# Performance work log

Measured on AMD Instinct MI355X. Metric: run time of the kernel, lower is better.

Reference implementation:

```python
import jax, jax.numpy as jnp
import numpy as np

B, S, D, H = 4, 2048, 512, 8
DK = D // H

def setup_inputs() -> dict:
    key = jax.random.key(0)
    ks = jax.random.split(key, 16)
    w = lambda i, shp: (jax.random.normal(ks[i], shp, jnp.float32) * 0.02)
    return {
        "q": jax.random.normal(ks[0], (B, S, D), jnp.float32),
        "k": jax.random.normal(ks[1], (B, S, D), jnp.float32),
        "v": jax.random.normal(ks[2], (B, S, D), jnp.float32),
        "mask": jax.random.randint(ks[3], (B, 1, S), 0, 2, jnp.int32),
        "Lexicon": jax.random.uniform(ks[4], (B, S), jnp.float32) * 1000.0,
        "Wq": w(5, (D, D)), "bq": w(6, (D,)),
        "Wk": w(7, (D, D)), "bk": w(8, (D,)),
        "Wv": w(9, (D, D)), "bv": w(10, (D,)),
        "Wo": w(11, (D, D)), "bo": w(12, (D,)),
        "Wl": w(13, (S, S)), "bl": w(14, (S,)),
    }

def reference(q, k, v, mask, Lexicon, Wq, bq, Wk, bk, Wv, bv, Wo, bo, Wl, bl):
    NEG = jnp.float32(-1e9)
    proj = lambda x, W, b: (x @ W + b).reshape(B, S, H, DK).transpose(0, 2, 1, 3)  # [B,H,S,DK]
    qh, kh, vh = proj(q, Wq, bq), proj(k, Wk, bk), proj(v, Wv, bv)
    scores = jnp.einsum('bhqd,bhkd->bhqk', qh, kh) / jnp.sqrt(jnp.float32(DK))  # [B,H,S,S]
    lex = (Lexicon / 1000.0) @ Wl + bl  # [B,S] lexicon bias over key positions
    m = mask[:, None, :, :] == 1  # [B,1,1,S]
    scores = jnp.where(m, NEG, scores)
    lexb = jnp.where(m, NEG, lex[:, None, None, :])  # [B,1,1,S]; broadcast over heads & queries
    # dropout in eval mode (identity); dual softmax then average
    attn = (jax.nn.softmax(scores, axis=-1) + jax.nn.softmax(lexb, axis=-1)) * 0.5
    out = jnp.einsum('bhqk,bhkd->bhqd', attn, vh)
    concat = out.transpose(0, 2, 1, 3).reshape(B, S, D)
    return concat @ Wo + bo
```

## Files before the change

kernel.cpp:

```cpp
#include <hip/hip_runtime.h>


typedef __attribute__((ext_vector_type(4))) float f32x4;
typedef __attribute__((ext_vector_type(8))) short s16x8;
typedef __attribute__((ext_vector_type(4))) short s16x4;

#define QSCALE 0.18033688011112042f

__device__ inline short f2bf(float f) {
  __bf16 h = (__bf16)f;
  return __builtin_bit_cast(short, h);
}
__device__ inline float fast_exp2(float x) {
#if __has_builtin(__builtin_amdgcn_exp2f)
  return __builtin_amdgcn_exp2f(x);
#else
  return exp2f(x);
#endif
}
__device__ inline void gl_lds16(const void* g, void* l) {
  __builtin_amdgcn_global_load_lds(
      (const __attribute__((address_space(1))) void*)g,
      (__attribute__((address_space(3))) void*)l, 16, 0, 0);
}

struct PrepArgs {
  const float* W[4];
  short* WT[4];
  const float* Lex;
  const float* Wl;
  float* part;
};

__global__ __launch_bounds__(256) void prep(PrepArgs pa) {
  const int blk = blockIdx.x;
  if (blk < 1024) {
    const int z = blk >> 8, tt = blk & 255;
    const float* __restrict__ W = pa.W[z];
    short* __restrict__ WT = pa.WT[z];
    const int n0 = (tt & 15) * 32, k0 = (tt >> 4) * 32;
    const int tx = threadIdx.x & 31, ty = threadIdx.x >> 5;
    __shared__ float Tl[32][33];
#pragma unroll
    for (int j = 0; j < 4; ++j)
      Tl[ty + j * 8][tx] = W[(size_t)(k0 + ty + j * 8) * 512 + n0 + tx];
    __syncthreads();
#pragma unroll
    for (int j = 0; j < 4; ++j) {
      int n = n0 + ty + j * 8, k = k0 + tx;
      int kg = k >> 3;
      int kswz = (((kg & ~7) | ((kg & 7) ^ (n & 7))) << 3) | (k & 7);
      WT[(size_t)n * 512 + kswz] = f2bf(Tl[tx][ty + j * 8]);
    }
  } else {
    const int jb = blk - 1024;
    const int j = (jb & 7) * 256 + threadIdx.x;
    const int sb = jb >> 3, s0 = sb * 128;
    __shared__ float Lsh[4][128];
#pragma unroll
    for (int l = 0; l < 2; ++l) {
      int idx = threadIdx.x + l * 256;
      Lsh[idx >> 7][idx & 127] = pa.Lex[(idx >> 7) * 2048 + s0 + (idx & 127)];
    }
    __syncthreads();
    float a0 = 0.f, a1 = 0.f, a2 = 0.f, a3 = 0.f;
#pragma unroll 4
    for (int si = 0; si < 128; ++si) {
      float w = pa.Wl[(size_t)(s0 + si) * 2048 + j];
      a0 += Lsh[0][si] * w; a1 += Lsh[1][si] * w;
      a2 += Lsh[2][si] * w; a3 += Lsh[3][si] * w;
    }
    pa.part[(sb * 4 + 0) * 2048 + j] = a0;
    pa.part[(sb * 4 + 1) * 2048 + j] = a1;
    pa.part[(sb * 4 + 2) * 2048 + j] = a2;
    pa.part[(sb * 4 + 3) * 2048 + j] = a3;
  }
}

__global__ __launch_bounds__(256) void plex_exp(const float* __restrict__ part,
                                                const float* __restrict__ bl,
                                                const int* __restrict__ mask,
                                                float* __restrict__ expv,
                                                float* __restrict__ psum) {
  const int b = blockIdx.x >> 3, jb = blockIdx.x & 7;
  const int j = jb * 256 + threadIdx.x;
  float s = 0.f;
#pragma unroll
  for (int sb = 0; sb < 16; ++sb) s += part[(sb * 4 + b) * 2048 + j];
  float vv = s * 0.001f + bl[j];
  float e = (mask[b * 2048 + j] == 1) ? 0.f : __expf(vv);
  expv[b * 2048 + j] = e;
  __shared__ float red[256];
  red[threadIdx.x] = e;
  __syncthreads();
  for (int off = 128; off; off >>= 1) {
    if (threadIdx.x < off) red[threadIdx.x] += red[threadIdx.x + off];
    __syncthreads();
  }
  if (threadIdx.x == 0) psum[b * 8 + jb] = red[0];
}

__global__ __launch_bounds__(256) void vbar1(const float* __restrict__ v,
                                             const float* __restrict__ expv,
                                             float* __restrict__ t1p) {
  const int blk = blockIdx.x;
  const int b = blk >> 6, kb = blk & 63;
  const int tid = threadIdx.x;
  float a0 = 0.f, a1 = 0.f;
#pragma unroll 4
  for (int kk = 0; kk < 32; ++kk) {
    int k = kb * 32 + kk;
    float e = expv[b * 2048 + k];
    const float* vr = v + (size_t)(b * 2048 + k) * 512;
    a0 += e * vr[tid];
    a1 += e * vr[tid + 256];
  }
  t1p[(size_t)blk * 512 + tid] = a0;
  t1p[(size_t)blk * 512 + tid + 256] = a1;
}

__global__ __launch_bounds__(256) void vbar2(const float* __restrict__ t1p,
                                             const float* __restrict__ psum,
                                             const float* __restrict__ Wv,
                                             const float* __restrict__ bv,
                                             float* __restrict__ vbar) {
  const int b = blockIdx.x, jb = blockIdx.y, tid = threadIdx.x;
  const int jl = tid & 63, sp = tid >> 6;
  const int j = jb * 64 + jl;
  __shared__ float t1[512];
  __shared__ float red[4][64];
#pragma unroll
  for (int l = 0; l < 2; ++l) {
    int idx = tid + l * 256;
    float s = 0.f;
#pragma unroll 8
    for (int p = 0; p < 64; ++p) s += t1p[(size_t)(b * 64 + p) * 512 + idx];
    t1[idx] = s;
  }
  __syncthreads();
  float a = 0.f;
#pragma unroll 4
  for (int d = sp * 128; d < sp * 128 + 128; ++d) a += t1[d] * Wv[(size_t)d * 512 + j];
  red[sp][jl] = a;
  __syncthreads();
  if (sp == 0) {
    float tot = 0.f;
#pragma unroll
    for (int p = 0; p < 8; ++p) tot += psum[b * 8 + p];
    float s = red[0][jl] + red[1][jl] + red[2][jl] + red[3][jl];
    vbar[b * 512 + j] = s / tot + bv[j];
  }
}

struct GemmArgs {
  const void* X[3];
  const short* WT[3];
  const float* bias[3];
  void* C[3];
  float oscale[3];
  int mode[3];
  const int* mask;
};

template <bool IN_F32>
__global__ __launch_bounds__(256) void gemm_fused(GemmArgs ga) {
  constexpr int LDA = IN_F32 ? 72 : 64;
  __shared__ alignas(16) short SH[64 * 72 + 128 * 64];
  short* Al = SH;
  short* Bl = SH + 64 * LDA;
  const int t = blockIdx.z;
  const short* __restrict__ WT = ga.WT[t];
  const float* __restrict__ bias = ga.bias[t];
  const int tid = threadIdx.x;
  const int lane = tid & 63, wid = tid >> 6;
  const int lr = lane & 15, lg = lane >> 4;
  const int wm = wid >> 1, wn = wid & 1;
  const int m0 = blockIdx.x * 64, n0 = blockIdx.y * 128;
  const int grow = lane >> 3, gch = lane & 7;

  f32x4 acc[2][4];
#pragma unroll
  for (int i = 0; i < 2; ++i)
#pragma unroll
    for (int j = 0; j < 4; ++j) acc[i][j] = {0.f, 0.f, 0.f, 0.f};

  for (int k0 = 0; k0 < 512; k0 += 64) {
    __syncthreads();
    if constexpr (IN_F32) {
      const float* X = (const float*)ga.X[t];
#pragma unroll
      for (int ii = 0; ii < 4; ++ii) {
        int fidx = tid + ii * 256;
        int row = fidx >> 4, kq = fidx & 15;
        f32x4 vv = *(const f32x4*)(X + (size_t)(m0 + row) * 512 + k0 + kq * 4);
        s16x4 hv = {f2bf(vv[0]), f2bf(vv[1]), f2bf(vv[2]), f2bf(vv[3])};
        *(s16x4*)(&Al[row * 72 + kq * 4]) = hv;
      }
    } else {
      const short* X = (const short*)ga.X[t];
#pragma unroll
      for (int c = 0; c < 2; ++c) {
        int r0 = wid * 16 + c * 8;
        int row = r0 + grow;
        gl_lds16(X + (size_t)(m0 + row) * 512 + k0 + ((gch ^ (row & 7)) << 3),
                 &Al[r0 * 64]);
      }
    }
#pragma unroll
    for (int c = 0; c < 4; ++c) {
      int r0 = wid * 32 + c * 8;
      int row = r0 + grow;
      gl_lds16(WT + (size_t)(n0 + row) * 512 + k0 + (gch << 3), &Bl[r0 * 64]);
    }
    __syncthreads();
#pragma unroll
    for (int ks = 0; ks < 2; ++ks) {
      s16x8 a[2], bfr[4];
#pragma unroll
      for (int mt = 0; mt < 2; ++mt) {
        int m = wm * 32 + mt * 16 + lr;
        if constexpr (IN_F32)
          a[mt] = *(const s16x8*)(&Al[m * 72 + ks * 32 + lg * 8]);
        else
          a[mt] = *(const s16x8*)(&Al[m * 64 + (((ks * 4 + lg) ^ (m & 7)) << 3)]);
      }
#pragma unroll
      for (int nt = 0; nt < 4; ++nt) {
        int n = wn * 64 + nt * 16 + lr;
        bfr[nt] = *(const s16x8*)(&Bl[n * 64 + (((ks * 4 + lg) ^ (n & 7)) << 3)]);
      }
#pragma unroll
      for (int mt = 0; mt < 2; ++mt)
#pragma unroll
        for (int nt = 0; nt < 4; ++nt)
          acc[mt][nt] = __builtin_amdgcn_mfma_f32_16x16x32_bf16(a[mt], bfr[nt],
                                                                acc[mt][nt], 0, 0, 0);
    }
  }
  const float os = ga.oscale[t];
  const int mode = ga.mode[t];
  if (mode == 1) {
    __syncthreads();
    short* Tt = SH;
#pragma unroll
    for (int nt = 0; nt < 4; ++nt) {
      int dl = wn * 64 + nt * 16 + lr;
      float bvv = bias[n0 + dl];
#pragma unroll
      for (int mt = 0; mt < 2; ++mt) {
        int sl = wm * 32 + mt * 16 + lg * 4;
#pragma unroll
        for (int i = 0; i < 4; ++i) {
          float mf = (ga.mask[m0 + sl + i] == 1) ? 0.f : 1.f;
          Tt[dl * 72 + sl + i] = f2bf((acc[mt][nt][i] + bvv) * mf);
        }
      }
    }
    __syncthreads();
    const int dl = tid >> 1, sh = (tid & 1) * 32;
    const int n = n0 + dl;
    const size_t base =
        ((size_t)((m0 >> 11) * 8 + (n >> 6)) * 64 + (n & 63)) * 2048 +
        (m0 & 2047) + sh;
#pragma unroll
    for (int c = 0; c < 4; ++c)
      *(s16x8*)((short*)ga.C[t] + base + c * 8) =
          *(const s16x8*)(&Tt[dl * 72 + sh + c * 8]);
  } else {
#pragma unroll
    for (int nt = 0; nt < 4; ++nt) {
      int col = n0 + wn * 64 + nt * 16 + lr;
      float bvv = bias[col];
#pragma unroll
      for (int mt = 0; mt < 2; ++mt) {
        int r0 = m0 + wm * 32 + mt * 16 + lg * 4;
        if (mode == 2) {
#pragma unroll
          for (int i = 0; i < 4; ++i)
            ((float*)ga.C[t])[(size_t)(r0 + i) * 512 + col] = acc[mt][nt][i] + bvv;
        } else {
#pragma unroll
          for (int i = 0; i < 4; ++i)
            ((short*)ga.C[t])[(size_t)(r0 + i) * 512 + col] =
                f2bf((acc[mt][nt][i] + bvv) * os);
        }
      }
    }
  }
}

__global__ __launch_bounds__(512) void flash_attn(const short* __restrict__ Qp,
                                                  const short* __restrict__ Kp,
                                                  const short* __restrict__ Vt,
                                                  const int* __restrict__ mask,
                                                  const float* __restrict__ vbar,
                                                  short* __restrict__ concat) {
  constexpr int S = 2048;
  __shared__ alignas(16) short Kl[2][64 * 72];
  __shared__ alignas(16) short Vl[2][64 * 72];
  __shared__ alignas(16) short Pl[8][16 * 72];
  __shared__ alignas(16) short Mb[2][64];
  const int id = blockIdx.x;
  const int xcd = id & 7, iw = id >> 3;
  const int bh = xcd * 4 + (iw >> 4), qb = iw & 15;
  const int b = bh >> 3, h = bh & 7;
  const int q0 = qb * 128;
  const int tid = threadIdx.x;
  const int lane = tid & 63, wid = tid >> 6;
  const int lr = lane & 15, lg = lane >> 4;

  const short* Qbase = Qp + ((size_t)(b * S) + q0 + wid * 16 + lr) * 512 + h * 64;
  const s16x8 aq0 = *(const s16x8*)(Qbase + lg * 8);
  const s16x8 aq1 = *(const s16x8*)(Qbase + 32 + lg * 8);

  const int srow = tid >> 3, sc = tid & 7;
  const short* Kg = Kp + ((size_t)(b * S) + srow) * 512 + h * 64 + sc * 8;
  const short* Vg = Vt + ((size_t)(bh * 64) + srow) * 2048 + sc * 8;

  s16x8 kreg = *(const s16x8*)(Kg);
  s16x8 vreg = *(const s16x8*)(Vg);
  *(s16x8*)(&Kl[0][srow * 72 + sc * 8]) = kreg;
  *(s16x8*)(&Vl[0][srow * 72 + sc * 8]) = vreg;
  if (tid < 64) Mb[0][tid] = (mask[b * S + tid] == 1) ? (short)0 : (short)0x3F80;
  __syncthreads();

  f32x4 acc[4];
#pragma unroll
  for (int i = 0; i < 4; ++i) acc[i] = {0.f, 0.f, 0.f, 0.f};
  f32x4 accL = {0.f, 0.f, 0.f, 0.f};
  const f32x4 zero = {0.f, 0.f, 0.f, 0.f};

  int cur = 0;
  for (int t = 0; t < 32; ++t) {
    const int nxt = cur ^ 1;
    int mnxt = 0;
    if (t < 31) {
      const size_t kv0n = (size_t)(t + 1) * 64;
      kreg = *(const s16x8*)(Kg + kv0n * 512);
      vreg = *(const s16x8*)(Vg + kv0n);
      if (tid < 64) mnxt = mask[b * S + kv0n + tid];
    }
    f32x4 st[4];
#pragma unroll
    for (int nt = 0; nt < 4; ++nt) {
      s16x8 k0f = *(const s16x8*)(&Kl[cur][(nt * 16 + lr) * 72 + lg * 8]);
      s16x8 k1f = *(const s16x8*)(&Kl[cur][(nt * 16 + lr) * 72 + 32 + lg * 8]);
      f32x4 tt = __builtin_amdgcn_mfma_f32_16x16x32_bf16(k0f, aq0, zero, 0, 0, 0);
      st[nt] = __builtin_amdgcn_mfma_f32_16x16x32_bf16(k1f, aq1, tt, 0, 0, 0);
    }
#pragma unroll
    for (int nt = 0; nt < 4; ++nt) {
      float p0 = fast_exp2(st[nt][0]);
      float p1 = fast_exp2(st[nt][1]);
      float p2 = fast_exp2(st[nt][2]);
      float p3 = fast_exp2(st[nt][3]);
      s16x4 pk = {f2bf(p0), f2bf(p1), f2bf(p2), f2bf(p3)};
      *(s16x4*)(&Pl[wid][lr * 72 + nt * 16 + lg * 4]) = pk;
    }
#pragma unroll
    for (int ks = 0; ks < 2; ++ks) {
      s16x8 ap = *(const s16x8*)(&Pl[wid][lr * 72 + ks * 32 + lg * 8]);
      s16x8 bm = *(const s16x8*)(&Mb[cur][ks * 32 + lg * 8]);
      accL = __builtin_amdgcn_mfma_f32_16x16x32_bf16(ap, bm, accL, 0, 0, 0);
#pragma unroll
      for (int dt = 0; dt < 4; ++dt) {
        s16x8 bv = *(const s16x8*)(&Vl[cur][(dt * 16 + lr) * 72 + ks * 32 + lg * 8]);
        acc[dt] = __builtin_amdgcn_mfma_f32_16x16x32_bf16(ap, bv, acc[dt], 0, 0, 0);
      }
    }
    if (t < 31) {
      *(s16x8*)(&Kl[nxt][srow * 72 + sc * 8]) = kreg;
      *(s16x8*)(&Vl[nxt][srow * 72 + sc * 8]) = vreg;
      if (tid < 64) Mb[nxt][tid] = (mnxt == 1) ? (short)0 : (short)0x3F80;
    }
    __syncthreads();
    cur = nxt;
  }
  f32x4 linv;
#pragma unroll
  for (int i = 0; i < 4; ++i) linv[i] = 0.5f / accL[i];
#pragma unroll
  for (int dt = 0; dt < 4; ++dt) {
    int d = dt * 16 + lr;
    float vb = 0.5f * vbar[bh * 64 + d];
#pragma unroll
    for (int i = 0; i < 4; ++i) {
      int q = q0 + wid * 16 + lg * 4 + i;
      concat[((size_t)(b * S) + q) * 512 + h * 64 + d] =
          f2bf(acc[dt][i] * linv[i] + vb);
    }
  }
}

extern "C" void kernel_launch(void* const* d_in, const int* in_sizes, int n_in,
                              void* d_out, int out_size, void* d_ws, size_t ws_size,
                              hipStream_t stream) {
  const float* q    = (const float*)d_in[0];
  const float* k    = (const float*)d_in[1];
  const float* v    = (const float*)d_in[2];
  const int*   mask = (const int*)d_in[3];
  const float* Lex  = (const float*)d_in[4];
  const float* Wq   = (const float*)d_in[5];
  const float* bq   = (const float*)d_in[6];
  const float* Wk   = (const float*)d_in[7];
  const float* bk   = (const float*)d_in[8];
  const float* Wv   = (const float*)d_in[9];
  const float* bv   = (const float*)d_in[10];
  const float* Wo   = (const float*)d_in[11];
  const float* bo   = (const float*)d_in[12];
  const float* Wl   = (const float*)d_in[13];
  const float* bl   = (const float*)d_in[14];
  float* out = (float*)d_out;

  char* ws = (char*)d_ws;
  const size_t TSZ = (size_t)8192 * 512 * 2;
  short* Qp  = (short*)(ws);
  short* Kp  = (short*)(ws + TSZ);
  short* Vtp = (short*)(ws + 2 * TSZ);
  short* Cc  = (short*)(ws + 3 * TSZ);
  float* part = (float*)(ws + 3 * TSZ);
  float* t1p  = (float*)(ws + 3 * TSZ + (512 << 10));
  short* WTq = (short*)(ws + 4 * TSZ);
  short* WTk = WTq + 512 * 512;
  short* WTv = WTk + 512 * 512;
  short* WTo = WTv + 512 * 512;
  float* expv  = (float*)(ws + 4 * TSZ + 4 * 512 * 512 * 2);
  float* psum  = expv + 4 * 2048;
  float* vbarp = psum + 64;

  PrepArgs pa;
  pa.W[0] = Wq; pa.W[1] = Wk; pa.W[2] = Wv; pa.W[3] = Wo;
  pa.WT[0] = WTq; pa.WT[1] = WTk; pa.WT[2] = WTv; pa.WT[3] = WTo;
  pa.Lex = Lex; pa.Wl = Wl; pa.part = part;
  prep<<<1152, 256, 0, stream>>>(pa);

  plex_exp<<<32, 256, 0, stream>>>(part, bl, mask, expv, psum);
  vbar1<<<256, 256, 0, stream>>>(v, expv, t1p);
  vbar2<<<dim3(4, 8), 256, 0, stream>>>(t1p, psum, Wv, bv, vbarp);

  GemmArgs gqkv;
  gqkv.X[0] = q;   gqkv.X[1] = k;   gqkv.X[2] = v;
  gqkv.WT[0] = WTq; gqkv.WT[1] = WTk; gqkv.WT[2] = WTv;
  gqkv.bias[0] = bq; gqkv.bias[1] = bk; gqkv.bias[2] = bv;
  gqkv.C[0] = Qp; gqkv.C[1] = Kp; gqkv.C[2] = Vtp;
  gqkv.oscale[0] = QSCALE; gqkv.oscale[1] = 1.f; gqkv.oscale[2] = 1.f;
  gqkv.mode[0] = 0; gqkv.mode[1] = 0; gqkv.mode[2] = 1;
  gqkv.mask = mask;
  gemm_fused<true><<<dim3(128, 4, 3), 256, 0, stream>>>(gqkv);

  flash_attn<<<512, 512, 0, stream>>>(Qp, Kp, Vtp, mask, vbarp, Cc);

  GemmArgs go;
  go.X[0] = Cc; go.WT[0] = WTo; go.bias[0] = bo; go.C[0] = out;
  go.oscale[0] = 1.f; go.mode[0] = 2;
  go.X[1] = nullptr; go.WT[1] = nullptr; go.bias[1] = nullptr; go.C[1] = nullptr;
  go.X[2] = nullptr; go.WT[2] = nullptr; go.bias[2] = nullptr; go.C[2] = nullptr;
  go.oscale[1] = go.oscale[2] = 1.f; go.mode[1] = go.mode[2] = 0;
  go.mask = mask;
  gemm_fused<false><<<dim3(128, 4, 1), 256, 0, stream>>>(go);
}
```

Before: 137.2 us.

## Fuse lexicon/vbar prep into QKV GEMM, widen GEMM N-tile, restructure flash attention

Removes the plex_exp and vbar1 kernels by running their work in an extra z-slice of the QKV GEMM launch, which cuts two launches and the expv round trip. GEMM tiles widen from 64x128 to 64x256, halving the grid and doubling per-block accumulators. Flash attention moves to 256-thread blocks that each process 32 query rows per wave, uses global_load_lds directly into XOR-swizzled unpadded LDS, and reuses K/V fragments across two query halves. The cost is higher register pressure and fewer blocks, which may lower occupancy.

```diff
diff --git a/kernel.cpp b/kernel.cpp
--- a/kernel.cpp
+++ b/kernel.cpp
@@ -77,50 +77,8 @@
   }
 }
 
-__global__ __launch_bounds__(256) void plex_exp(const float* __restrict__ part,
-                                                const float* __restrict__ bl,
-                                                const int* __restrict__ mask,
-                                                float* __restrict__ expv,
-                                                float* __restrict__ psum) {
-  const int b = blockIdx.x >> 3, jb = blockIdx.x & 7;
-  const int j = jb * 256 + threadIdx.x;
-  float s = 0.f;
-#pragma unroll
-  for (int sb = 0; sb < 16; ++sb) s += part[(sb * 4 + b) * 2048 + j];
-  float vv = s * 0.001f + bl[j];
-  float e = (mask[b * 2048 + j] == 1) ? 0.f : __expf(vv);
-  expv[b * 2048 + j] = e;
-  __shared__ float red[256];
-  red[threadIdx.x] = e;
-  __syncthreads();
-  for (int off = 128; off; off >>= 1) {
-    if (threadIdx.x < off) red[threadIdx.x] += red[threadIdx.x + off];
-    __syncthreads();
-  }
-  if (threadIdx.x == 0) psum[b * 8 + jb] = red[0];
-}
-
-__global__ __launch_bounds__(256) void vbar1(const float* __restrict__ v,
-                                             const float* __restrict__ expv,
-                                             float* __restrict__ t1p) {
-  const int blk = blockIdx.x;
-  const int b = blk >> 6, kb = blk & 63;
-  const int tid = threadIdx.x;
-  float a0 = 0.f, a1 = 0.f;
-#pragma unroll 4
-  for (int kk = 0; kk < 32; ++kk) {
-    int k = kb * 32 + kk;
-    float e = expv[b * 2048 + k];
-    const float* vr = v + (size_t)(b * 2048 + k) * 512;
-    a0 += e * vr[tid];
-    a1 += e * vr[tid + 256];
-  }
-  t1p[(size_t)blk * 512 + tid] = a0;
-  t1p[(size_t)blk * 512 + tid + 256] = a1;
-}
-
 __global__ __launch_bounds__(256) void vbar2(const float* __restrict__ t1p,
-                                             const float* __restrict__ psum,
+                                             const float* __restrict__ psp,
                                              const float* __restrict__ Wv,
                                              const float* __restrict__ bv,
                                              float* __restrict__ vbar) {
@@ -145,8 +103,8 @@
   __syncthreads();
   if (sp == 0) {
     float tot = 0.f;
-#pragma unroll
-    for (int p = 0; p < 8; ++p) tot += psum[b * 8 + p];
+#pragma unroll 8
+    for (int p = 0; p < 64; ++p) tot += psp[b * 64 + p];
     float s = red[0][jl] + red[1][jl] + red[2][jl] + red[3][jl];
     vbar[b * 512 + j] = s / tot + bv[j];
   }
@@ -160,29 +118,65 @@
   float oscale[3];
   int mode[3];
   const int* mask;
+  const float* part;
+  const float* bl;
+  const float* vsrc;
+  float* t1p;
+  float* psp;
 };
 
 template <bool IN_F32>
 __global__ __launch_bounds__(256) void gemm_fused(GemmArgs ga) {
+  __shared__ alignas(16) short SH[64 * 72 + 256 * 64];
+  const int tid = threadIdx.x;
+
+  if (blockIdx.z == 3) {
+    float* ek = (float*)SH;
+    const int id2 = blockIdx.y * 128 + blockIdx.x;
+    const int b = id2 >> 6, kb = id2 & 63;
+    if (tid < 32) {
+      int k = kb * 32 + tid;
+      float s = 0.f;
+#pragma unroll
+      for (int sb = 0; sb < 16; ++sb) s += ga.part[(sb * 4 + b) * 2048 + k];
+      float lx = s * 0.001f + ga.bl[k];
+      ek[tid] = (ga.mask[b * 2048 + k] == 1) ? 0.f : __expf(lx);
+    }
+    __syncthreads();
+    float a0 = 0.f, a1 = 0.f;
+#pragma unroll 4
+    for (int kk = 0; kk < 32; ++kk) {
+      float e = ek[kk];
+      const float* vr = ga.vsrc + (size_t)(b * 2048 + kb * 32 + kk) * 512;
+      a0 += e * vr[tid];
+      a1 += e * vr[tid + 256];
+    }
+    ga.t1p[(size_t)id2 * 512 + tid] = a0;
+    ga.t1p[(size_t)id2 * 512 + tid + 256] = a1;
+    if (tid == 0) {
+      float s = 0.f;
+      for (int i = 0; i < 32; ++i) s += ek[i];
+      ga.psp[id2] = s;
+    }
+    return;
+  }
+
   constexpr int LDA = IN_F32 ? 72 : 64;
-  __shared__ alignas(16) short SH[64 * 72 + 128 * 64];
   short* Al = SH;
   short* Bl = SH + 64 * LDA;
   const int t = blockIdx.z;
   const short* __restrict__ WT = ga.WT[t];
   const float* __restrict__ bias = ga.bias[t];
-  const int tid = threadIdx.x;
   const int lane = tid & 63, wid = tid >> 6;
   const int lr = lane & 15, lg = lane >> 4;
   const int wm = wid >> 1, wn = wid & 1;
-  const int m0 = blockIdx.x * 64, n0 = blockIdx.y * 128;
-  const int grow = lane >> 3, gch = lane & 7;
-
-  f32x4 acc[2][4];
+  const int m0 = blockIdx.x * 64, n0 = blockIdx.y * 256;
+
+  f32x4 acc[2][8];
 #pragma unroll
   for (int i = 0; i < 2; ++i)
 #pragma unroll
-    for (int j = 0; j < 4; ++j) acc[i][j] = {0.f, 0.f, 0.f, 0.f};
+    for (int j = 0; j < 8; ++j) acc[i][j] = {0.f, 0.f, 0.f, 0.f};
 
   for (int k0 = 0; k0 < 512; k0 += 64) {
     __syncthreads();
@@ -200,22 +194,22 @@
       const short* X = (const short*)ga.X[t];
 #pragma unroll
       for (int c = 0; c < 2; ++c) {
-        int r0 = wid * 16 + c * 8;
-        int row = r0 + grow;
-        gl_lds16(X + (size_t)(m0 + row) * 512 + k0 + ((gch ^ (row & 7)) << 3),
-                 &Al[r0 * 64]);
-      }
-    }
-#pragma unroll
-    for (int c = 0; c < 4; ++c) {
-      int r0 = wid * 32 + c * 8;
-      int row = r0 + grow;
-      gl_lds16(WT + (size_t)(n0 + row) * 512 + k0 + (gch << 3), &Bl[r0 * 64]);
+        int u = c * 256 + tid;
+        int row = u >> 3, g = u & 7;
+        gl_lds16(X + (size_t)(m0 + row) * 512 + k0 + ((g ^ (row & 7)) << 3),
+                 &Al[u * 8]);
+      }
+    }
+#pragma unroll
+    for (int c = 0; c < 8; ++c) {
+      int u = c * 256 + tid;
+      int row = u >> 3, g = u & 7;
+      gl_lds16(WT + (size_t)(n0 + row) * 512 + k0 + (g << 3), &Bl[u * 8]);
     }
     __syncthreads();
 #pragma unroll
     for (int ks = 0; ks < 2; ++ks) {
-      s16x8 a[2], bfr[4];
+      s16x8 a[2], bfr[8];
 #pragma unroll
       for (int mt = 0; mt < 2; ++mt) {
         int m = wm * 32 + mt * 16 + lr;
@@ -225,14 +219,14 @@
           a[mt] = *(const s16x8*)(&Al[m * 64 + (((ks * 4 + lg) ^ (m & 7)) << 3)]);
       }
 #pragma unroll
-      for (int nt = 0; nt < 4; ++nt) {
-        int n = wn * 64 + nt * 16 + lr;
+      for (int nt = 0; nt < 8; ++nt) {
+        int n = wn * 128 + nt * 16 + lr;
         bfr[nt] = *(const s16x8*)(&Bl[n * 64 + (((ks * 4 + lg) ^ (n & 7)) << 3)]);
       }
 #pragma unroll
       for (int mt = 0; mt < 2; ++mt)
 #pragma unroll
-        for (int nt = 0; nt < 4; ++nt)
+        for (int nt = 0; nt < 8; ++nt)
           acc[mt][nt] = __builtin_amdgcn_mfma_f32_16x16x32_bf16(a[mt], bfr[nt],
                                                                 acc[mt][nt], 0, 0, 0);
     }
@@ -243,8 +237,8 @@
     __syncthreads();
     short* Tt = SH;
 #pragma unroll
-    for (int nt = 0; nt < 4; ++nt) {
-      int dl = wn * 64 + nt * 16 + lr;
+    for (int nt = 0; nt < 8; ++nt) {
+      int dl = wn * 128 + nt * 16 + lr;
       float bvv = bias[n0 + dl];
 #pragma unroll
       for (int mt = 0; mt < 2; ++mt) {
@@ -257,19 +251,16 @@
       }
     }
     __syncthreads();
-    const int dl = tid >> 1, sh = (tid & 1) * 32;
-    const int n = n0 + dl;
+    const int n = n0 + tid;
     const size_t base =
-        ((size_t)((m0 >> 11) * 8 + (n >> 6)) * 64 + (n & 63)) * 2048 +
-        (m0 & 2047) + sh;
-#pragma unroll
-    for (int c = 0; c < 4; ++c)
-      *(s16x8*)((short*)ga.C[t] + base + c * 8) =
-          *(const s16x8*)(&Tt[dl * 72 + sh + c * 8]);
+        ((size_t)((m0 >> 11) * 8 + (n >> 6)) * 64 + (n & 63)) * 2048 + (m0 & 2047);
+#pragma unroll
+    for (int c = 0; c < 8; ++c)
+      *(s16x8*)((short*)ga.C[t] + base + c * 8) = *(const s16x8*)(&Tt[tid * 72 + c * 8]);
   } else {
 #pragma unroll
-    for (int nt = 0; nt < 4; ++nt) {
-      int col = n0 + wn * 64 + nt * 16 + lr;
+    for (int nt = 0; nt < 8; ++nt) {
+      int col = n0 + wn * 128 + nt * 16 + lr;
       float bvv = bias[col];
 #pragma unroll
       for (int mt = 0; mt < 2; ++mt) {
@@ -289,16 +280,16 @@
   }
 }
 
-__global__ __launch_bounds__(512) void flash_attn(const short* __restrict__ Qp,
+__global__ __launch_bounds__(256) void flash_attn(const short* __restrict__ Qp,
                                                   const short* __restrict__ Kp,
                                                   const short* __restrict__ Vt,
                                                   const int* __restrict__ mask,
                                                   const float* __restrict__ vbar,
                                                   short* __restrict__ concat) {
   constexpr int S = 2048;
-  __shared__ alignas(16) short Kl[2][64 * 72];
-  __shared__ alignas(16) short Vl[2][64 * 72];
-  __shared__ alignas(16) short Pl[8][16 * 72];
+  __shared__ alignas(16) short Kl[2][64 * 64];
+  __shared__ alignas(16) short Vl[2][64 * 64];
+  __shared__ alignas(16) short Pl[4][32 * 64];
   __shared__ alignas(16) short Mb[2][64];
   const int id = blockIdx.x;
   const int xcd = id & 7, iw = id >> 3;
@@ -309,26 +300,35 @@
   const int lane = tid & 63, wid = tid >> 6;
   const int lr = lane & 15, lg = lane >> 4;
 
-  const short* Qbase = Qp + ((size_t)(b * S) + q0 + wid * 16 + lr) * 512 + h * 64;
-  const s16x8 aq0 = *(const s16x8*)(Qbase + lg * 8);
-  const s16x8 aq1 = *(const s16x8*)(Qbase + 32 + lg * 8);
-
-  const int srow = tid >> 3, sc = tid & 7;
-  const short* Kg = Kp + ((size_t)(b * S) + srow) * 512 + h * 64 + sc * 8;
-  const short* Vg = Vt + ((size_t)(bh * 64) + srow) * 2048 + sc * 8;
-
-  s16x8 kreg = *(const s16x8*)(Kg);
-  s16x8 vreg = *(const s16x8*)(Vg);
-  *(s16x8*)(&Kl[0][srow * 72 + sc * 8]) = kreg;
-  *(s16x8*)(&Vl[0][srow * 72 + sc * 8]) = vreg;
+  const int row0 = tid >> 3, row1 = (tid + 256) >> 3, sg = tid & 7;
+  const short* Kg0 = Kp + ((size_t)(b * S) + row0) * 512 + h * 64 + ((sg ^ (row0 & 7)) << 3);
+  const short* Kg1 = Kp + ((size_t)(b * S) + row1) * 512 + h * 64 + ((sg ^ (row1 & 7)) << 3);
+  const short* Vg0 = Vt + ((size_t)(bh * 64) + row0) * 2048 + ((sg ^ (row0 & 7)) << 3);
+  const short* Vg1 = Vt + ((size_t)(bh * 64) + row1) * 2048 + ((sg ^ (row1 & 7)) << 3);
+
+  gl_lds16(Kg0, &Kl[0][tid * 8]);
+  gl_lds16(Kg1, &Kl[0][(tid + 256) * 8]);
+  gl_lds16(Vg0, &Vl[0][tid * 8]);
+  gl_lds16(Vg1, &Vl[0][(tid + 256) * 8]);
   if (tid < 64) Mb[0][tid] = (mask[b * S + tid] == 1) ? (short)0 : (short)0x3F80;
+
+  const short* Qb0 = Qp + ((size_t)(b * S) + q0 + wid * 32 + lr) * 512 + h * 64;
+  s16x8 aq0[2], aq1[2];
+#pragma unroll
+  for (int qh = 0; qh < 2; ++qh) {
+    aq0[qh] = *(const s16x8*)(Qb0 + (size_t)qh * 16 * 512 + lg * 8);
+    aq1[qh] = *(const s16x8*)(Qb0 + (size_t)qh * 16 * 512 + 32 + lg * 8);
+  }
+
+  f32x4 acc[2][4];
+#pragma unroll
+  for (int qh = 0; qh < 2; ++qh)
+#pragma unroll
+    for (int i = 0; i < 4; ++i) acc[qh][i] = {0.f, 0.f, 0.f, 0.f};
+  f32x4 accL[2] = {{0.f, 0.f, 0.f, 0.f}, {0.f, 0.f, 0.f, 0.f}};
+  const f32x4 zero = {0.f, 0.f, 0.f, 0.f};
+
   __syncthreads();
-
-  f32x4 acc[4];
-#pragma unroll
-  for (int i = 0; i < 4; ++i) acc[i] = {0.f, 0.f, 0.f, 0.f};
-  f32x4 accL = {0.f, 0.f, 0.f, 0.f};
-  const f32x4 zero = {0.f, 0.f, 0.f, 0.f};
 
   int cur = 0;
   for (int t = 0; t < 32; ++t) {
@@ -336,58 +336,76 @@
     int mnxt = 0;
     if (t < 31) {
       const size_t kv0n = (size_t)(t + 1) * 64;
-      kreg = *(const s16x8*)(Kg + kv0n * 512);
-      vreg = *(const s16x8*)(Vg + kv0n);
+      gl_lds16(Kg0 + kv0n * 512, &Kl[nxt][tid * 8]);
+      gl_lds16(Kg1 + kv0n * 512, &Kl[nxt][(tid + 256) * 8]);
+      gl_lds16(Vg0 + kv0n, &Vl[nxt][tid * 8]);
+      gl_lds16(Vg1 + kv0n, &Vl[nxt][(tid + 256) * 8]);
       if (tid < 64) mnxt = mask[b * S + kv0n + tid];
     }
-    f32x4 st[4];
+    f32x4 st[2][4];
 #pragma unroll
     for (int nt = 0; nt < 4; ++nt) {
-      s16x8 k0f = *(const s16x8*)(&Kl[cur][(nt * 16 + lr) * 72 + lg * 8]);
-      s16x8 k1f = *(const s16x8*)(&Kl[cur][(nt * 16 + lr) * 72 + 32 + lg * 8]);
-      f32x4 tt = __builtin_amdgcn_mfma_f32_16x16x32_bf16(k0f, aq0, zero, 0, 0, 0);
-      st[nt] = __builtin_amdgcn_mfma_f32_16x16x32_bf16(k1f, aq1, tt, 0, 0, 0);
-    }
-#pragma unroll
-    for (int nt = 0; nt < 4; ++nt) {
-      float p0 = fast_exp2(st[nt][0]);
-      float p1 = fast_exp2(st[nt][1]);
-      float p2 = fast_exp2(st[nt][2]);
-      float p3 = fast_exp2(st[nt][3]);
-      s16x4 pk = {f2bf(p0), f2bf(p1), f2bf(p2), f2bf(p3)};
-      *(s16x4*)(&Pl[wid][lr * 72 + nt * 16 + lg * 4]) = pk;
+      const int rbase = (nt * 16 + lr) * 64;
+      s16x8 k0f = *(const s16x8*)(&Kl[cur][rbase + ((lg ^ (lr & 7)) << 3)]);
+      s16x8 k1f = *(const s16x8*)(&Kl[cur][rbase + (((4 + lg) ^ (lr & 7)) << 3)]);
+#pragma unroll
+      for (int qh = 0; qh < 2; ++qh) {
+        f32x4 tt = __builtin_amdgcn_mfma_f32_16x16x32_bf16(k0f, aq0[qh], zero, 0, 0, 0);
+        st[qh][nt] = __builtin_amdgcn_mfma_f32_16x16x32_bf16(k1f, aq1[qh], tt, 0, 0, 0);
+      }
+    }
+#pragma unroll
+    for (int qh = 0; qh < 2; ++qh) {
+      const int prow = (qh * 16 + lr) * 64;
+#pragma unroll
+      for (int nt = 0; nt < 4; ++nt) {
+        float p0 = fast_exp2(st[qh][nt][0]);
+        float p1 = fast_exp2(st[qh][nt][1]);
+        float p2 = fast_exp2(st[qh][nt][2]);
+        float p3 = fast_exp2(st[qh][nt][3]);
+        s16x4 pk = {f2bf(p0), f2bf(p1), f2bf(p2), f2bf(p3)};
+        int g = nt * 2 + (lg >> 1);
+        *(s16x4*)(&Pl[wid][prow + ((g ^ (lr & 7)) << 3) + ((lg & 1) << 2)]) = pk;
+      }
     }
 #pragma unroll
     for (int ks = 0; ks < 2; ++ks) {
-      s16x8 ap = *(const s16x8*)(&Pl[wid][lr * 72 + ks * 32 + lg * 8]);
+      const int fg = (((ks * 4 + lg) ^ (lr & 7)) << 3);
       s16x8 bm = *(const s16x8*)(&Mb[cur][ks * 32 + lg * 8]);
-      accL = __builtin_amdgcn_mfma_f32_16x16x32_bf16(ap, bm, accL, 0, 0, 0);
+      s16x8 ap[2];
+#pragma unroll
+      for (int qh = 0; qh < 2; ++qh) {
+        ap[qh] = *(const s16x8*)(&Pl[wid][(qh * 16 + lr) * 64 + fg]);
+        accL[qh] = __builtin_amdgcn_mfma_f32_16x16x32_bf16(ap[qh], bm, accL[qh], 0, 0, 0);
+      }
 #pragma unroll
       for (int dt = 0; dt < 4; ++dt) {
-        s16x8 bv = *(const s16x8*)(&Vl[cur][(dt * 16 + lr) * 72 + ks * 32 + lg * 8]);
-        acc[dt] = __builtin_amdgcn_mfma_f32_16x16x32_bf16(ap, bv, acc[dt], 0, 0, 0);
-      }
-    }
-    if (t < 31) {
-      *(s16x8*)(&Kl[nxt][srow * 72 + sc * 8]) = kreg;
-      *(s16x8*)(&Vl[nxt][srow * 72 + sc * 8]) = vreg;
-      if (tid < 64) Mb[nxt][tid] = (mnxt == 1) ? (short)0 : (short)0x3F80;
-    }
+        s16x8 bv = *(const s16x8*)(&Vl[cur][(dt * 16 + lr) * 64 + fg]);
+#pragma unroll
+        for (int qh = 0; qh < 2; ++qh)
+          acc[qh][dt] = __builtin_amdgcn_mfma_f32_16x16x32_bf16(ap[qh], bv, acc[qh][dt], 0, 0, 0);
+      }
+    }
+    if (t < 31 && tid < 64)
+      Mb[nxt][tid] = (mnxt == 1) ? (short)0 : (short)0x3F80;
     __syncthreads();
     cur = nxt;
   }
-  f32x4 linv;
-#pragma unroll
-  for (int i = 0; i < 4; ++i) linv[i] = 0.5f / accL[i];
-#pragma unroll
-  for (int dt = 0; dt < 4; ++dt) {
-    int d = dt * 16 + lr;
-    float vb = 0.5f * vbar[bh * 64 + d];
-#pragma unroll
-    for (int i = 0; i < 4; ++i) {
-      int q = q0 + wid * 16 + lg * 4 + i;
-      concat[((size_t)(b * S) + q) * 512 + h * 64 + d] =
-          f2bf(acc[dt][i] * linv[i] + vb);
+#pragma unroll
+  for (int qh = 0; qh < 2; ++qh) {
+    f32x4 linv;
+#pragma unroll
+    for (int i = 0; i < 4; ++i) linv[i] = 0.5f / accL[qh][i];
+#pragma unroll
+    for (int dt = 0; dt < 4; ++dt) {
+      int d = dt * 16 + lr;
+      float vb = 0.5f * vbar[bh * 64 + d];
+#pragma unroll
+      for (int i = 0; i < 4; ++i) {
+        int q = q0 + wid * 32 + qh * 16 + lg * 4 + i;
+        concat[((size_t)(b * S) + q) * 512 + h * 64 + d] =
+            f2bf(acc[qh][dt][i] * linv[i] + vb);
+      }
     }
   }
 }
@@ -424,19 +442,14 @@
   short* WTk = WTq + 512 * 512;
   short* WTv = WTk + 512 * 512;
   short* WTo = WTv + 512 * 512;
-  float* expv  = (float*)(ws + 4 * TSZ + 4 * 512 * 512 * 2);
-  float* psum  = expv + 4 * 2048;
-  float* vbarp = psum + 64;
+  float* psp   = (float*)(ws + 4 * TSZ + 4 * 512 * 512 * 2);
+  float* vbarp = psp + 256;
 
   PrepArgs pa;
   pa.W[0] = Wq; pa.W[1] = Wk; pa.W[2] = Wv; pa.W[3] = Wo;
   pa.WT[0] = WTq; pa.WT[1] = WTk; pa.WT[2] = WTv; pa.WT[3] = WTo;
   pa.Lex = Lex; pa.Wl = Wl; pa.part = part;
   prep<<<1152, 256, 0, stream>>>(pa);
-
-  plex_exp<<<32, 256, 0, stream>>>(part, bl, mask, expv, psum);
-  vbar1<<<256, 256, 0, stream>>>(v, expv, t1p);
-  vbar2<<<dim3(4, 8), 256, 0, stream>>>(t1p, psum, Wv, bv, vbarp);
 
   GemmArgs gqkv;
   gqkv.X[0] = q;   gqkv.X[1] = k;   gqkv.X[2] = v;
@@ -446,9 +459,13 @@
   gqkv.oscale[0] = QSCALE; gqkv.oscale[1] = 1.f; gqkv.oscale[2] = 1.f;
   gqkv.mode[0] = 0; gqkv.mode[1] = 0; gqkv.mode[2] = 1;
   gqkv.mask = mask;
-  gemm_fused<true><<<dim3(128, 4, 3), 256, 0, stream>>>(gqkv);
-
-  flash_attn<<<512, 512, 0, stream>>>(Qp, Kp, Vtp, mask, vbarp, Cc);
+  gqkv.part = part; gqkv.bl = bl; gqkv.vsrc = v;
+  gqkv.t1p = t1p; gqkv.psp = psp;
+  gemm_fused<true><<<dim3(128, 2, 4), 256, 0, stream>>>(gqkv);
+
+  vbar2<<<dim3(4, 8), 256, 0, stream>>>(t1p, psp, Wv, bv, vbarp);
+
+  flash_attn<<<512, 256, 0, stream>>>(Qp, Kp, Vtp, mask, vbarp, Cc);
 
   GemmArgs go;
   go.X[0] = Cc; go.WT[0] = WTo; go.bias[0] = bo; go.C[0] = out;
@@ -457,5 +474,7 @@
   go.X[2] = nullptr; go.WT[2] = nullptr; go.bias[2] = nullptr; go.C[2] = nullptr;
   go.oscale[1] = go.oscale[2] = 1.f; go.mode[1] = go.mode[2] = 0;
   go.mask = mask;
-  gemm_fused<false><<<dim3(128, 4, 1), 256, 0, stream>>>(go);
-}
+  go.part = nullptr; go.bl = nullptr; go.vsrc = nullptr;
+  go.t1p = nullptr; go.psp = nullptr;
+  gemm_fused<false><<<dim3(128, 2, 1), 256, 0, stream>>>(go);
+}
```

Result: faster. 134.2 us (-2.2%).
